# Optimization experiments

Measured on AMD Instinct MI355X. Metric: run time of the kernel, lower is better.

Reference implementation:

```python
import jax, jax.numpy as jnp
import numpy as np

N_NODES = 100000
N_EDGES = 1600000
IN_F = 512
OUT_F = 256
ORDER = 2


def setup_inputs() -> dict:
    key = jax.random.key(0)
    k1, k2, k3, k4, k5 = jax.random.split(key, 5)
    features = jax.random.normal(k1, (N_NODES, IN_F), dtype=jnp.float32)
    # Xavier-uniform init like torch.nn.init.xavier_uniform_
    limit = float(np.sqrt(6.0 / (IN_F + OUT_F)))
    weight = jax.random.uniform(k2, (IN_F, OUT_F), dtype=jnp.float32, minval=-limit, maxval=limit)
    row = jnp.sort(jax.random.randint(k3, (N_EDGES,), 0, N_NODES, dtype=jnp.int32))
    col = jax.random.randint(k4, (N_EDGES,), 0, N_NODES, dtype=jnp.int32)
    adj_vals = jax.random.uniform(k5, (N_EDGES,), dtype=jnp.float32)
    return {"features": features, "weight": weight, "row": row, "col": col, "adj_vals": adj_vals}


def _spmm(row, col, vals, x, n):
    # out[i] = sum_{e: row[e]==i} vals[e] * x[col[e]]  (COO sparse @ dense)
    msgs = vals[:, None] * x[col]  # [E, F]
    return jax.ops.segment_sum(msgs, row, num_segments=n)


def reference(features, weight, row, col, adj_vals):
    out = jnp.tanh(features @ weight)  # dense mm + tanh (active=True)
    for _ in range(ORDER):  # spmm once, then order-1 more times
        out = _spmm(row, col, adj_vals, out, N_NODES)
    return out
```

## Files before the change

kernel.cpp:

```cpp
#include <hip/hip_runtime.h>
#include <hip/hip_bf16.h>

#define M_NODES 100000
#define N_EDGES 1600000
#define K_IN 512
#define N_OUT 256

typedef short bf16x8 __attribute__((ext_vector_type(8)));
typedef float f32x4 __attribute__((ext_vector_type(4)));

#define GLOBAL_AS __attribute__((address_space(1)))
#define LDS_AS __attribute__((address_space(3)))

__device__ inline unsigned short f2bf_u(float f) {
  union { float f; unsigned u; } x; x.f = f;
  unsigned r = x.u + 0x7FFFu + ((x.u >> 16) & 1u);
  return (unsigned short)(r >> 16);
}
__device__ inline float bfu2f(unsigned short h) {
  union { unsigned u; float f; } x; x.u = ((unsigned)h) << 16;
  return x.f;
}

__global__ void prep_w_kernel(const float* __restrict__ w, short* __restrict__ wt) {
  int idx = blockIdx.x * 256 + threadIdx.x;
  int k = idx >> 8, n = idx & 255;
  wt[n * K_IN + k] = (short)f2bf_u(w[idx]);
}

__global__ void build_rp_kernel(const int* __restrict__ row, int* __restrict__ rp) {
  int r = blockIdx.x * 256 + threadIdx.x;
  if (r > M_NODES) return;
  int lo = 0, hi = N_EDGES;
  while (lo < hi) {
    int mid = (lo + hi) >> 1;
    if (row[mid] < r) lo = mid + 1; else hi = mid;
  }
  rp[r] = lo;
}

__global__ __launch_bounds__(256) void gemm_tanh_kernel(
    const float* __restrict__ A, const short* __restrict__ Wt,
    unsigned short* __restrict__ H) {
  __shared__ __align__(16) short As[64 * 64];
  __shared__ __align__(16) short Bs[256 * 64];
  const int tid = threadIdx.x;
  const int wave = tid >> 6, lane = tid & 63;
  const int quad = lane >> 4, l16 = lane & 15;
  const int row0 = blockIdx.x * 64;

  f32x4 acc[16];
  #pragma unroll
  for (int i = 0; i < 16; ++i) acc[i] = (f32x4){0.f, 0.f, 0.f, 0.f};

  const int ra = tid >> 2;
  const int kb = (tid & 3) << 4;
  const int gr = min(row0 + ra, M_NODES - 1);
  const float* Arow = A + (size_t)gr * K_IN;

  for (int k0 = 0; k0 < K_IN; k0 += 64) {
    #pragma unroll
    for (int it = 0; it < 8; ++it) {
      int g = wave * 512 + it * 64 + lane;
      int n = g >> 3, phys = g & 7;
      int j = phys ^ (n & 7);
      const short* gp = Wt + (size_t)n * K_IN + k0 + j * 8;
      __builtin_amdgcn_global_load_lds(
          (GLOBAL_AS const void*)gp,
          (LDS_AS void*)&Bs[(wave * 512 + it * 64) * 8],
          16, 0, 0);
    }
    float4 a0 = *(const float4*)&Arow[k0 + kb];
    float4 a1 = *(const float4*)&Arow[k0 + kb + 4];
    float4 a2 = *(const float4*)&Arow[k0 + kb + 8];
    float4 a3 = *(const float4*)&Arow[k0 + kb + 12];
    union { unsigned short s[16]; int4 v[2]; } u;
    u.s[0]=f2bf_u(a0.x); u.s[1]=f2bf_u(a0.y); u.s[2]=f2bf_u(a0.z); u.s[3]=f2bf_u(a0.w);
    u.s[4]=f2bf_u(a1.x); u.s[5]=f2bf_u(a1.y); u.s[6]=f2bf_u(a1.z); u.s[7]=f2bf_u(a1.w);
    u.s[8]=f2bf_u(a2.x); u.s[9]=f2bf_u(a2.y); u.s[10]=f2bf_u(a2.z); u.s[11]=f2bf_u(a2.w);
    u.s[12]=f2bf_u(a3.x); u.s[13]=f2bf_u(a3.y); u.s[14]=f2bf_u(a3.z); u.s[15]=f2bf_u(a3.w);
    int lc0 = kb >> 3;
    #pragma unroll
    for (int c = 0; c < 2; ++c) {
      int phys = (lc0 + c) ^ (ra & 7);
      *(int4*)&As[ra * 64 + phys * 8] = u.v[c];
    }
    __syncthreads();
    const int r = wave * 16 + l16;
    #pragma unroll
    for (int kstep = 0; kstep < 2; ++kstep) {
      int lc = kstep * 4 + quad;
      bf16x8 af = *(const bf16x8*)&As[r * 64 + (lc ^ (r & 7)) * 8];
      #pragma unroll
      for (int nt = 0; nt < 16; ++nt) {
        int n = nt * 16 + l16;
        bf16x8 bfr = *(const bf16x8*)&Bs[n * 64 + (lc ^ (n & 7)) * 8];
        acc[nt] = __builtin_amdgcn_mfma_f32_16x16x32_bf16(af, bfr, acc[nt], 0, 0, 0);
      }
    }
    __syncthreads();
  }
  #pragma unroll
  for (int nt = 0; nt < 16; ++nt) {
    #pragma unroll
    for (int rr = 0; rr < 4; ++rr) {
      int row = row0 + wave * 16 + quad * 4 + rr;
      if (row < M_NODES) {
        H[(size_t)row * N_OUT + nt * 16 + l16] = f2bf_u(tanhf(acc[nt][rr]));
      }
    }
  }
}

__global__ __launch_bounds__(256) void spmm_bf_bf(
    const int* __restrict__ rp, const int* __restrict__ colv,
    const float* __restrict__ vals, const unsigned short* __restrict__ x,
    unsigned short* __restrict__ y) {
  int w = (blockIdx.x * 256 + threadIdx.x) >> 6;
  int lane = threadIdx.x & 63;
  int i = __builtin_amdgcn_readfirstlane(w);
  int s = rp[i], e = rp[i + 1];
  float a0 = 0.f, a1 = 0.f, a2 = 0.f, a3 = 0.f;
  for (int t = s; t < e; ++t) {
    float v = vals[t];
    int c = colv[t];
    ushort4 xv = *(const ushort4*)(x + (size_t)c * N_OUT + lane * 4);
    a0 += v * bfu2f(xv.x); a1 += v * bfu2f(xv.y);
    a2 += v * bfu2f(xv.z); a3 += v * bfu2f(xv.w);
  }
  ushort4 o;
  o.x = f2bf_u(a0); o.y = f2bf_u(a1); o.z = f2bf_u(a2); o.w = f2bf_u(a3);
  *(ushort4*)(y + (size_t)i * N_OUT + lane * 4) = o;
}

__global__ __launch_bounds__(256) void spmm_bf_f32(
    const int* __restrict__ rp, const int* __restrict__ colv,
    const float* __restrict__ vals, const unsigned short* __restrict__ x,
    float* __restrict__ y) {
  int w = (blockIdx.x * 256 + threadIdx.x) >> 6;
  int lane = threadIdx.x & 63;
  int i = __builtin_amdgcn_readfirstlane(w);
  int s = rp[i], e = rp[i + 1];
  float a0 = 0.f, a1 = 0.f, a2 = 0.f, a3 = 0.f;
  for (int t = s; t < e; ++t) {
    float v = vals[t];
    int c = colv[t];
    ushort4 xv = *(const ushort4*)(x + (size_t)c * N_OUT + lane * 4);
    a0 += v * bfu2f(xv.x); a1 += v * bfu2f(xv.y);
    a2 += v * bfu2f(xv.z); a3 += v * bfu2f(xv.w);
  }
  float4 o = {a0, a1, a2, a3};
  *(float4*)(y + (size_t)i * N_OUT + lane * 4) = o;
}

extern "C" void kernel_launch(void* const* d_in, const int* in_sizes, int n_in,
                              void* d_out, int out_size, void* d_ws, size_t ws_size,
                              hipStream_t stream) {
  const float* features = (const float*)d_in[0];
  const float* weight   = (const float*)d_in[1];
  const int*   row      = (const int*)d_in[2];
  const int*   col      = (const int*)d_in[3];
  const float* vals     = (const float*)d_in[4];
  float* out = (float*)d_out;

  char* ws = (char*)d_ws;
  const size_t HB = (size_t)M_NODES * N_OUT * 2;
  const size_t RPB = 400016;
  unsigned short* H  = (unsigned short*)ws;
  unsigned short* y1 = (unsigned short*)(ws + HB);
  int*   rp = (int*)(ws + 2 * HB);
  short* Wt = (short*)(ws + 2 * HB + RPB);

  prep_w_kernel<<<512, 256, 0, stream>>>(weight, Wt);
  build_rp_kernel<<<(M_NODES + 1 + 255) / 256, 256, 0, stream>>>(row, rp);
  gemm_tanh_kernel<<<(M_NODES + 63) / 64, 256, 0, stream>>>(features, Wt, H);
  spmm_bf_bf<<<25000, 256, 0, stream>>>(rp, col, vals, H, y1);
  spmm_bf_f32<<<25000, 256, 0, stream>>>(rp, col, vals, y1, out);
}
```

Baseline: 628.8 us.

## Enlarge GEMM row tile to 128 and batch SpMM edge loads via readlane

The GEMM now computes 128 rows per block, with each wave handling two 16-row MFMA groups. Each B fragment read from LDS is therefore reused twice, which halves the W tile reloads per output row. The SpMM kernels now load 64 col/val entries cooperatively across lanes and broadcast them with readlane. They also unroll the gather by four so several row loads are in flight at once instead of serially dependent scalar loads. The costs are more accumulator registers in the GEMM, which may lower occupancy, and half as many GEMM blocks.

```diff
diff --git a/kernel.cpp b/kernel.cpp
--- a/kernel.cpp
+++ b/kernel.cpp
@@ -42,19 +42,21 @@
 __global__ __launch_bounds__(256) void gemm_tanh_kernel(
     const float* __restrict__ A, const short* __restrict__ Wt,
     unsigned short* __restrict__ H) {
-  __shared__ __align__(16) short As[64 * 64];
+  __shared__ __align__(16) short As[128 * 64];
   __shared__ __align__(16) short Bs[256 * 64];
   const int tid = threadIdx.x;
   const int wave = tid >> 6, lane = tid & 63;
   const int quad = lane >> 4, l16 = lane & 15;
-  const int row0 = blockIdx.x * 64;
-
-  f32x4 acc[16];
+  const int row0 = blockIdx.x * 128;
+
+  f32x4 acc[2][16];
   #pragma unroll
-  for (int i = 0; i < 16; ++i) acc[i] = (f32x4){0.f, 0.f, 0.f, 0.f};
-
-  const int ra = tid >> 2;
-  const int kb = (tid & 3) << 4;
+  for (int g = 0; g < 2; ++g)
+    #pragma unroll
+    for (int i = 0; i < 16; ++i) acc[g][i] = (f32x4){0.f, 0.f, 0.f, 0.f};
+
+  const int ra = tid >> 1;
+  const int kh = (tid & 1) << 5;
   const int gr = min(row0 + ra, M_NODES - 1);
   const float* Arow = A + (size_t)gr * K_IN;
 
@@ -70,87 +72,112 @@
           (LDS_AS void*)&Bs[(wave * 512 + it * 64) * 8],
           16, 0, 0);
     }
-    float4 a0 = *(const float4*)&Arow[k0 + kb];
-    float4 a1 = *(const float4*)&Arow[k0 + kb + 4];
-    float4 a2 = *(const float4*)&Arow[k0 + kb + 8];
-    float4 a3 = *(const float4*)&Arow[k0 + kb + 12];
-    union { unsigned short s[16]; int4 v[2]; } u;
-    u.s[0]=f2bf_u(a0.x); u.s[1]=f2bf_u(a0.y); u.s[2]=f2bf_u(a0.z); u.s[3]=f2bf_u(a0.w);
-    u.s[4]=f2bf_u(a1.x); u.s[5]=f2bf_u(a1.y); u.s[6]=f2bf_u(a1.z); u.s[7]=f2bf_u(a1.w);
-    u.s[8]=f2bf_u(a2.x); u.s[9]=f2bf_u(a2.y); u.s[10]=f2bf_u(a2.z); u.s[11]=f2bf_u(a2.w);
-    u.s[12]=f2bf_u(a3.x); u.s[13]=f2bf_u(a3.y); u.s[14]=f2bf_u(a3.z); u.s[15]=f2bf_u(a3.w);
-    int lc0 = kb >> 3;
-    #pragma unroll
-    for (int c = 0; c < 2; ++c) {
-      int phys = (lc0 + c) ^ (ra & 7);
-      *(int4*)&As[ra * 64 + phys * 8] = u.v[c];
+    #pragma unroll
+    for (int half = 0; half < 2; ++half) {
+      const float* p = &Arow[k0 + kh + half * 16];
+      float4 b0 = *(const float4*)(p);
+      float4 b1 = *(const float4*)(p + 4);
+      float4 b2 = *(const float4*)(p + 8);
+      float4 b3 = *(const float4*)(p + 12);
+      union { unsigned short s[16]; int4 v[2]; } u;
+      u.s[0]=f2bf_u(b0.x); u.s[1]=f2bf_u(b0.y); u.s[2]=f2bf_u(b0.z); u.s[3]=f2bf_u(b0.w);
+      u.s[4]=f2bf_u(b1.x); u.s[5]=f2bf_u(b1.y); u.s[6]=f2bf_u(b1.z); u.s[7]=f2bf_u(b1.w);
+      u.s[8]=f2bf_u(b2.x); u.s[9]=f2bf_u(b2.y); u.s[10]=f2bf_u(b2.z); u.s[11]=f2bf_u(b2.w);
+      u.s[12]=f2bf_u(b3.x); u.s[13]=f2bf_u(b3.y); u.s[14]=f2bf_u(b3.z); u.s[15]=f2bf_u(b3.w);
+      int lc0 = (kh + half * 16) >> 3;
+      #pragma unroll
+      for (int c = 0; c < 2; ++c) {
+        int phys = (lc0 + c) ^ (ra & 7);
+        *(int4*)&As[ra * 64 + phys * 8] = u.v[c];
+      }
     }
     __syncthreads();
-    const int r = wave * 16 + l16;
+    const int m0 = wave * 32 + l16;
+    const int m1 = m0 + 16;
     #pragma unroll
     for (int kstep = 0; kstep < 2; ++kstep) {
       int lc = kstep * 4 + quad;
-      bf16x8 af = *(const bf16x8*)&As[r * 64 + (lc ^ (r & 7)) * 8];
+      bf16x8 af0 = *(const bf16x8*)&As[m0 * 64 + (lc ^ (m0 & 7)) * 8];
+      bf16x8 af1 = *(const bf16x8*)&As[m1 * 64 + (lc ^ (m1 & 7)) * 8];
       #pragma unroll
       for (int nt = 0; nt < 16; ++nt) {
         int n = nt * 16 + l16;
         bf16x8 bfr = *(const bf16x8*)&Bs[n * 64 + (lc ^ (n & 7)) * 8];
-        acc[nt] = __builtin_amdgcn_mfma_f32_16x16x32_bf16(af, bfr, acc[nt], 0, 0, 0);
+        acc[0][nt] = __builtin_amdgcn_mfma_f32_16x16x32_bf16(af0, bfr, acc[0][nt], 0, 0, 0);
+        acc[1][nt] = __builtin_amdgcn_mfma_f32_16x16x32_bf16(af1, bfr, acc[1][nt], 0, 0, 0);
       }
     }
     __syncthreads();
   }
   #pragma unroll
-  for (int nt = 0; nt < 16; ++nt) {
-    #pragma unroll
-    for (int rr = 0; rr < 4; ++rr) {
-      int row = row0 + wave * 16 + quad * 4 + rr;
-      if (row < M_NODES) {
-        H[(size_t)row * N_OUT + nt * 16 + l16] = f2bf_u(tanhf(acc[nt][rr]));
+  for (int g = 0; g < 2; ++g) {
+    #pragma unroll
+    for (int nt = 0; nt < 16; ++nt) {
+      #pragma unroll
+      for (int rr = 0; rr < 4; ++rr) {
+        int row = row0 + wave * 32 + g * 16 + quad * 4 + rr;
+        if (row < M_NODES) {
+          H[(size_t)row * N_OUT + nt * 16 + l16] = f2bf_u(tanhf(acc[g][nt][rr]));
+        }
       }
     }
   }
 }
 
-__global__ __launch_bounds__(256) void spmm_bf_bf(
+template <typename OutT>
+__global__ __launch_bounds__(256) void spmm_kernel_t(
     const int* __restrict__ rp, const int* __restrict__ colv,
     const float* __restrict__ vals, const unsigned short* __restrict__ x,
-    unsigned short* __restrict__ y) {
+    OutT* __restrict__ y) {
   int w = (blockIdx.x * 256 + threadIdx.x) >> 6;
   int lane = threadIdx.x & 63;
   int i = __builtin_amdgcn_readfirstlane(w);
   int s = rp[i], e = rp[i + 1];
   float a0 = 0.f, a1 = 0.f, a2 = 0.f, a3 = 0.f;
-  for (int t = s; t < e; ++t) {
-    float v = vals[t];
-    int c = colv[t];
-    ushort4 xv = *(const ushort4*)(x + (size_t)c * N_OUT + lane * 4);
-    a0 += v * bfu2f(xv.x); a1 += v * bfu2f(xv.y);
-    a2 += v * bfu2f(xv.z); a3 += v * bfu2f(xv.w);
-  }
-  ushort4 o;
-  o.x = f2bf_u(a0); o.y = f2bf_u(a1); o.z = f2bf_u(a2); o.w = f2bf_u(a3);
-  *(ushort4*)(y + (size_t)i * N_OUT + lane * 4) = o;
-}
-
-__global__ __launch_bounds__(256) void spmm_bf_f32(
-    const int* __restrict__ rp, const int* __restrict__ colv,
-    const float* __restrict__ vals, const unsigned short* __restrict__ x,
-    float* __restrict__ y) {
-  int w = (blockIdx.x * 256 + threadIdx.x) >> 6;
-  int lane = threadIdx.x & 63;
-  int i = __builtin_amdgcn_readfirstlane(w);
-  int s = rp[i], e = rp[i + 1];
-  float a0 = 0.f, a1 = 0.f, a2 = 0.f, a3 = 0.f;
-  for (int t = s; t < e; ++t) {
-    float v = vals[t];
-    int c = colv[t];
-    ushort4 xv = *(const ushort4*)(x + (size_t)c * N_OUT + lane * 4);
-    a0 += v * bfu2f(xv.x); a1 += v * bfu2f(xv.y);
-    a2 += v * bfu2f(xv.z); a3 += v * bfu2f(xv.w);
-  }
-  float4 o = {a0, a1, a2, a3};
-  *(float4*)(y + (size_t)i * N_OUT + lane * 4) = o;
+  for (int base = s; base < e; base += 64) {
+    int t = base + lane;
+    int cl = 0; unsigned vl = 0;
+    if (t < e) { cl = colv[t]; vl = __builtin_bit_cast(unsigned, vals[t]); }
+    int cnt = min(64, e - base);
+    int j = 0;
+    for (; j + 4 <= cnt; j += 4) {
+      int c0 = __builtin_amdgcn_readlane(cl, j);
+      int c1 = __builtin_amdgcn_readlane(cl, j + 1);
+      int c2 = __builtin_amdgcn_readlane(cl, j + 2);
+      int c3 = __builtin_amdgcn_readlane(cl, j + 3);
+      float v0 = __builtin_bit_cast(float, __builtin_amdgcn_readlane(vl, j));
+      float v1 = __builtin_bit_cast(float, __builtin_amdgcn_readlane(vl, j + 1));
+      float v2 = __builtin_bit_cast(float, __builtin_amdgcn_readlane(vl, j + 2));
+      float v3 = __builtin_bit_cast(float, __builtin_amdgcn_readlane(vl, j + 3));
+      ushort4 x0 = *(const ushort4*)(x + (size_t)c0 * N_OUT + lane * 4);
+      ushort4 x1 = *(const ushort4*)(x + (size_t)c1 * N_OUT + lane * 4);
+      ushort4 x2 = *(const ushort4*)(x + (size_t)c2 * N_OUT + lane * 4);
+      ushort4 x3 = *(const ushort4*)(x + (size_t)c3 * N_OUT + lane * 4);
+      a0 += v0 * bfu2f(x0.x); a1 += v0 * bfu2f(x0.y);
+      a2 += v0 * bfu2f(x0.z); a3 += v0 * bfu2f(x0.w);
+      a0 += v1 * bfu2f(x1.x); a1 += v1 * bfu2f(x1.y);
+      a2 += v1 * bfu2f(x1.z); a3 += v1 * bfu2f(x1.w);
+      a0 += v2 * bfu2f(x2.x); a1 += v2 * bfu2f(x2.y);
+      a2 += v2 * bfu2f(x2.z); a3 += v2 * bfu2f(x2.w);
+      a0 += v3 * bfu2f(x3.x); a1 += v3 * bfu2f(x3.y);
+      a2 += v3 * bfu2f(x3.z); a3 += v3 * bfu2f(x3.w);
+    }
+    for (; j < cnt; ++j) {
+      int c = __builtin_amdgcn_readlane(cl, j);
+      float v = __builtin_bit_cast(float, __builtin_amdgcn_readlane(vl, j));
+      ushort4 xv = *(const ushort4*)(x + (size_t)c * N_OUT + lane * 4);
+      a0 += v * bfu2f(xv.x); a1 += v * bfu2f(xv.y);
+      a2 += v * bfu2f(xv.z); a3 += v * bfu2f(xv.w);
+    }
+  }
+  if constexpr (sizeof(OutT) == 2) {
+    ushort4 o;
+    o.x = f2bf_u(a0); o.y = f2bf_u(a1); o.z = f2bf_u(a2); o.w = f2bf_u(a3);
+    *(ushort4*)((unsigned short*)y + (size_t)i * N_OUT + lane * 4) = o;
+  } else {
+    float4 o = {a0, a1, a2, a3};
+    *(float4*)((float*)y + (size_t)i * N_OUT + lane * 4) = o;
+  }
 }
 
 extern "C" void kernel_launch(void* const* d_in, const int* in_sizes, int n_in,
@@ -173,7 +200,7 @@
 
   prep_w_kernel<<<512, 256, 0, stream>>>(weight, Wt);
   build_rp_kernel<<<(M_NODES + 1 + 255) / 256, 256, 0, stream>>>(row, rp);
-  gemm_tanh_kernel<<<(M_NODES + 63) / 64, 256, 0, stream>>>(features, Wt, H);
-  spmm_bf_bf<<<25000, 256, 0, stream>>>(rp, col, vals, H, y1);
-  spmm_bf_f32<<<25000, 256, 0, stream>>>(rp, col, vals, y1, out);
-}
+  gemm_tanh_kernel<<<(M_NODES + 127) / 128, 256, 0, stream>>>(features, Wt, H);
+  spmm_kernel_t<unsigned short><<<25000, 256, 0, stream>>>(rp, col, vals, H, y1);
+  spmm_kernel_t<float><<<25000, 256, 0, stream>>>(rp, col, vals, y1, out);
+}
```

Result: slower. 673.6 us (+7.1%).
